# Optimization experiments

Measured on AMD Instinct MI355X. Metric: run time of the kernel, lower is better.

The kernel has to match this reference:

```python
import jax, jax.numpy as jnp
import numpy as np

B, T, DIM, E, H = 128, 512, 256, 512, 512

def _linear_params(key, out_dim, in_dim, bias=True):
    k1, k2 = jax.random.split(key)
    bound = 1.0 / np.sqrt(in_dim)
    W = jax.random.uniform(k1, (out_dim, in_dim), jnp.float32, -bound, bound)
    if bias:
        b = jax.random.uniform(k2, (out_dim,), jnp.float32, -bound, bound)
        return W, b
    return W

def setup_inputs() -> dict:
    key = jax.random.key(0)
    ks = jax.random.split(key, 12)
    x_t = jax.random.normal(ks[0], (B, T, DIM), jnp.float32)
    h0 = jax.random.normal(ks[1], (B, H), jnp.float32)
    c0 = jax.random.normal(ks[2], (B, H), jnp.float32)
    We, be = _linear_params(ks[3], E, DIM)
    Wf, bf = _linear_params(ks[4], H, E)   # forget input proj
    Wi, bi = _linear_params(ks[5], H, E)   # input gate
    Wg, bg = _linear_params(ks[6], H, E)   # cell candidate
    Wo, bo = _linear_params(ks[7], H, E)   # output gate
    Rf = _linear_params(ks[8], H, H, bias=False)
    Ri = _linear_params(ks[9], H, H, bias=False)
    Rg = _linear_params(ks[10], H, H, bias=False)
    Ro = _linear_params(ks[11], H, H, bias=False)
    return dict(x_t=x_t, h0=h0, c0=c0, We=We, be=be,
                Wf=Wf, bf=bf, Wi=Wi, bi=bi, Wg=Wg, bg=bg, Wo=Wo, bo=bo,
                Rf=Rf, Ri=Ri, Rg=Rg, Ro=Ro)

def reference(x_t, h0, c0, We, be, Wf, bf, Wi, bi, Wg, bg, Wo, bo, Rf, Ri, Rg, Ro):
    # Embedding: [B,T,DIM] -> [B,T,E]
    xe = jnp.einsum('btd,ed->bte', x_t, We) + be
    # Batch all input-to-hidden projections across time in one GEMM each.
    xf = jnp.einsum('bte,he->bth', xe, Wf) + bf
    xi = jnp.einsum('bte,he->bth', xe, Wi) + bi
    xg = jnp.einsum('bte,he->bth', xe, Wg) + bg
    xo = jnp.einsum('bte,he->bth', xe, Wo) + bo
    xs = jnp.stack([xi, xf, xg, xo], axis=0)  # [4,B,T,H]

    def step(carry, x4):
        h, c = carry
        xi_t, xf_t, xg_t, xo_t = x4
        i = jax.nn.sigmoid(xi_t + h @ Ri.T)
        f = jax.nn.sigmoid(xf_t + h @ Rf.T)
        g = jnp.tanh(xg_t + h @ Rg.T)
        c_next = g * i + f * c
        o = jax.nn.sigmoid(xo_t + h @ Ro.T)
        h_next = o * jnp.tanh(c_next)
        return (h_next, c_next), h_next

    (h_last, c_last), hs = jax.lax.scan(step, (h0, c0), jnp.moveaxis(xs, 2, 0))
    hidden_seq = jnp.swapaxes(hs, 0, 1)  # [B,T,H]
    return hidden_seq, h_last, c_last
```

## Files before the change

### kernel.cpp

```cpp
#include <hip/hip_runtime.h>
#include <hip/hip_bf16.h>

#define B_ 128
#define T_ 512
#define DIM_ 256
#define E_ 512
#define H_ 512
#define NB_ 32
#define NG_ 8
#define WROW 1032

typedef __attribute__((ext_vector_type(8))) short short8;
typedef __attribute__((ext_vector_type(4))) float floatx4;
typedef unsigned long long ull_t;

__device__ __forceinline__ float sigmoidf_(float x) {
  return 1.0f / (1.0f + __expf(-x));
}

__device__ __forceinline__ short f2bs(float f) {
  __hip_bfloat16 h = __float2bfloat16(f);
  return *reinterpret_cast<short*>(&h);
}

__global__ __launch_bounds__(256) void cvt_we(const float* __restrict__ src,
                                              __hip_bfloat16* __restrict__ dst,
                                              int n) {
  int i = blockIdx.x * 256 + threadIdx.x;
  if (i < n) dst[i] = __float2bfloat16(src[i]);
}

__global__ __launch_bounds__(256) void embed_gemm(
    const float* __restrict__ A,
    const __hip_bfloat16* __restrict__ W,
    const float* __restrict__ bias,
    __hip_bfloat16* __restrict__ C)
{
  const int tid = threadIdx.x;
  const int lane = tid & 63;
  const int w = tid >> 6;
  const int q = lane >> 4;
  const int l15 = lane & 15;
  const int m0 = blockIdx.x * 32 + (w >> 1) * 16;
  const int n0 = (w & 1) * 256;

  const float* a_base = A + (size_t)(m0 + l15) * DIM_ + q * 8;

  floatx4 acc[16];
#pragma unroll
  for (int j = 0; j < 16; ++j) acc[j] = (floatx4){0.f, 0.f, 0.f, 0.f};

  for (int ks = 0; ks < 8; ++ks) {
    const float* ap = a_base + ks * 32;
    short8 a;
#pragma unroll
    for (int j = 0; j < 8; ++j) a[j] = f2bs(ap[j]);
    short8 bf[16];
#pragma unroll
    for (int j = 0; j < 16; ++j) {
      const short* b_ptr =
          (const short*)W + (n0 + j * 16 + l15) * DIM_ + ks * 32 + q * 8;
      bf[j] = *(const short8*)b_ptr;
    }
#pragma unroll
    for (int j = 0; j < 16; ++j)
      acc[j] = __builtin_amdgcn_mfma_f32_16x16x32_bf16(a, bf[j], acc[j], 0, 0, 0);
  }

#pragma unroll
  for (int j = 0; j < 16; ++j) {
    const int col = n0 + j * 16 + l15;
    const float bv = bias[col];
#pragma unroll
    for (int r = 0; r < 4; ++r) {
      const int row = m0 + q * 4 + r;
      C[(size_t)row * E_ + col] = __float2bfloat16(acc[j][r] + bv);
    }
  }
}

__global__ __launch_bounds__(256, 1) void lstm_persist(
    const float* __restrict__ h0,
    const float* __restrict__ c0,
    const float* __restrict__ Wi_, const float* __restrict__ bi_,
    const float* __restrict__ Wf_, const float* __restrict__ bf_,
    const float* __restrict__ Wg_, const float* __restrict__ bg_,
    const float* __restrict__ Wo_, const float* __restrict__ bo_,
    const float* __restrict__ Ri_, const float* __restrict__ Rf_,
    const float* __restrict__ Rg_, const float* __restrict__ Ro_,
    const __hip_bfloat16* __restrict__ xe,
    unsigned* __restrict__ hbuf32,
    unsigned* __restrict__ seq,
    float* __restrict__ out)
{
  extern __shared__ short wts[];
  __shared__ float pbuf[4][4][16][17];
  __shared__ float cbuf[16][16];
  __shared__ float bias_s[4][16];

  const int tid = threadIdx.x;
  const int lane = tid & 63;
  const int w = tid >> 6;
  const int q = lane >> 4;
  const int l15 = lane & 15;
  const int blk = blockIdx.x;
  const int g = blk & 7;
  const int jb = blk >> 3;
  const int b0 = g * 16;
  const int d0 = jb * 16;
  unsigned* seq_g = seq + g * NB_;
  ull_t* hbuf64 = (ull_t*)hbuf32;

  const float* Wp[4] = {Wi_, Wf_, Wg_, Wo_};
  const float* Rp[4] = {Ri_, Rf_, Rg_, Ro_};
  const float* bp[4] = {bi_, bf_, bg_, bo_};

  for (int idx = tid; idx < 64 * 128; idx += 256) {
    const int row = idx >> 7;
    const int ch = idx & 127;
    const int G = row >> 4, dl = row & 15;
    const int k = ch * 8;
    const float* src = (k < 512) ? Wp[G] + (d0 + dl) * E_ + k
                                 : Rp[G] + (d0 + dl) * H_ + (k - 512);
    short8 v;
#pragma unroll
    for (int s = 0; s < 8; ++s) v[s] = f2bs(src[s]);
    *(short8*)&wts[row * WROW + k] = v;
  }
  if (tid < 64) {
    const int G = tid >> 4, n = tid & 15;
    bias_s[G][n] = bp[G][d0 + n];
  }
  {
    const int m = tid >> 4, n = tid & 15;
    cbuf[m][n] = c0[(b0 + m) * H_ + d0 + n];
  }
  if (tid < 128) {
    const int u = g * 4096 + jb * 128 + tid;
    unsigned pk = (unsigned)(unsigned short)f2bs(h0[2 * u]) |
                  ((unsigned)(unsigned short)f2bs(h0[2 * u + 1]) << 16);
    __hip_atomic_store(&hbuf32[u], pk, __ATOMIC_RELAXED,
                       __HIP_MEMORY_SCOPE_AGENT);
  }

  __syncthreads();
  if (tid == 0)
    __hip_atomic_store(&seq_g[jb], 1u, __ATOMIC_RELAXED,
                       __HIP_MEMORY_SCOPE_AGENT);

  const short* xbase = (const short*)xe +
      (size_t)(b0 + l15) * T_ * E_ + w * 256 + q * 8;

  const int lds_base = l15 * WROW + w * 256 + q * 8;

  short8 cur[8];
  if (w < 2) {
#pragma unroll
    for (int s = 0; s < 8; ++s) cur[s] = *(const short8*)(xbase + s * 32);
    floatx4 acc[4];
#pragma unroll
    for (int G = 0; G < 4; ++G) acc[G] = (floatx4){0.f, 0.f, 0.f, 0.f};
#pragma unroll
    for (int s = 0; s < 8; ++s)
#pragma unroll
      for (int G = 0; G < 4; ++G) {
        short8 bfr = *(const short8*)&wts[G * 16 * WROW + lds_base + s * 32];
        acc[G] = __builtin_amdgcn_mfma_f32_16x16x32_bf16(cur[s], bfr, acc[G], 0, 0, 0);
      }
#pragma unroll
    for (int G = 0; G < 4; ++G)
#pragma unroll
      for (int r = 0; r < 4; ++r)
        pbuf[w][G][q * 4 + r][l15] = acc[G][r];
#pragma unroll
    for (int s = 0; s < 8; ++s) cur[s] = *(const short8*)(xbase + E_ + s * 32);
  }

  for (int t = 0; t < T_; ++t) {
    if (w >= 2) {
      const unsigned tgt = (unsigned)(t + 1);
      for (;;) {
        unsigned v = __hip_atomic_load(&seq_g[lane & 31], __ATOMIC_RELAXED,
                                       __HIP_MEMORY_SCOPE_AGENT);
        if (__all((int)(v >= tgt))) break;
      }
      const ull_t* hb = hbuf64 + (size_t)(t & 1) * (B_ * H_ / 4) +
                        (b0 + l15) * (H_ / 4) + (w - 2) * 64 + q * 2;
      short8 hc[8];
#pragma unroll
      for (int s = 0; s < 8; ++s) {
        union { ull_t u[2]; short8 v8; } uu;
        uu.u[0] = __hip_atomic_load(hb + s * 8, __ATOMIC_RELAXED,
                                    __HIP_MEMORY_SCOPE_AGENT);
        uu.u[1] = __hip_atomic_load(hb + s * 8 + 1, __ATOMIC_RELAXED,
                                    __HIP_MEMORY_SCOPE_AGENT);
        hc[s] = uu.v8;
      }
      floatx4 acc[4];
#pragma unroll
      for (int G = 0; G < 4; ++G) acc[G] = (floatx4){0.f, 0.f, 0.f, 0.f};
#pragma unroll
      for (int s = 0; s < 8; ++s)
#pragma unroll
        for (int G = 0; G < 4; ++G) {
          short8 bfr = *(const short8*)&wts[G * 16 * WROW + lds_base + s * 32];
          acc[G] = __builtin_amdgcn_mfma_f32_16x16x32_bf16(hc[s], bfr, acc[G], 0, 0, 0);
        }
#pragma unroll
      for (int G = 0; G < 4; ++G)
#pragma unroll
        for (int r = 0; r < 4; ++r)
          pbuf[w][G][q * 4 + r][l15] = acc[G][r];
    }
    __syncthreads();

    const int m = tid >> 4, n = tid & 15;
    float pre[4];
#pragma unroll
    for (int G = 0; G < 4; ++G)
      pre[G] = pbuf[0][G][m][n] + pbuf[1][G][m][n] + pbuf[2][G][m][n] +
               pbuf[3][G][m][n] + bias_s[G][n];
    const float iv = sigmoidf_(pre[0]);
    const float fv = sigmoidf_(pre[1]);
    const float gv = tanhf(pre[2]);
    const float ov = sigmoidf_(pre[3]);
    const float c = gv * iv + fv * cbuf[m][n];
    cbuf[m][n] = c;
    const float hval = ov * tanhf(c);

    {
      unsigned hv = (unsigned)(unsigned short)f2bs(hval);
      unsigned ov2 = __shfl_xor(hv, 1);
      if ((n & 1) == 0) {
        unsigned pk = hv | (ov2 << 16);
        __hip_atomic_store(
            &hbuf32[((t + 1) & 1) * (B_ * H_ / 2) + (b0 + m) * (H_ / 2) +
                    ((d0 + n) >> 1)],
            pk, __ATOMIC_RELAXED, __HIP_MEMORY_SCOPE_AGENT);
      }
    }
    __syncthreads();
    if (tid == 0)
      __hip_atomic_store(&seq_g[jb], (unsigned)(t + 2), __ATOMIC_RELAXED,
                         __HIP_MEMORY_SCOPE_AGENT);

    out[((size_t)(b0 + m) * T_ + t) * H_ + d0 + n] = hval;
    if (t == T_ - 1) {
      out[(size_t)B_ * T_ * H_ + (b0 + m) * H_ + d0 + n] = hval;
      out[(size_t)B_ * T_ * H_ + B_ * H_ + (b0 + m) * H_ + d0 + n] = c;
    }

    if (w < 2 && t + 1 < T_) {
      floatx4 acc[4];
#pragma unroll
      for (int G = 0; G < 4; ++G) acc[G] = (floatx4){0.f, 0.f, 0.f, 0.f};
#pragma unroll
      for (int s = 0; s < 8; ++s)
#pragma unroll
        for (int G = 0; G < 4; ++G) {
          short8 bfr = *(const short8*)&wts[G * 16 * WROW + lds_base + s * 32];
          acc[G] = __builtin_amdgcn_mfma_f32_16x16x32_bf16(cur[s], bfr, acc[G], 0, 0, 0);
        }
#pragma unroll
      for (int G = 0; G < 4; ++G)
#pragma unroll
        for (int r = 0; r < 4; ++r)
          pbuf[w][G][q * 4 + r][l15] = acc[G][r];
      if (t + 2 < T_) {
        const short* xp = xbase + (size_t)(t + 2) * E_;
#pragma unroll
        for (int s = 0; s < 8; ++s) cur[s] = *(const short8*)(xp + s * 32);
      }
    }
  }
}

extern "C" void kernel_launch(void* const* d_in, const int* in_sizes, int n_in,
                              void* d_out, int out_size, void* d_ws,
                              size_t ws_size, hipStream_t stream) {
  const float* x_t = (const float*)d_in[0];
  const float* h0  = (const float*)d_in[1];
  const float* c0  = (const float*)d_in[2];
  const float* We  = (const float*)d_in[3];
  const float* be  = (const float*)d_in[4];
  const float* Wf  = (const float*)d_in[5];
  const float* bf_ = (const float*)d_in[6];
  const float* Wi  = (const float*)d_in[7];
  const float* bi  = (const float*)d_in[8];
  const float* Wg  = (const float*)d_in[9];
  const float* bg  = (const float*)d_in[10];
  const float* Wo  = (const float*)d_in[11];
  const float* bo  = (const float*)d_in[12];
  const float* Rf  = (const float*)d_in[13];
  const float* Ri  = (const float*)d_in[14];
  const float* Rg  = (const float*)d_in[15];
  const float* Ro  = (const float*)d_in[16];
  float* out = (float*)d_out;

  char* ws = (char*)d_ws;
  unsigned* seq  = (unsigned*)ws;
  unsigned* hbuf = (unsigned*)(ws + 4096);
  __hip_bfloat16* Web  = (__hip_bfloat16*)(ws + 4096 + 262144);
  __hip_bfloat16* xe   = (__hip_bfloat16*)(ws + 4096 + 2 * 262144);

  hipMemsetAsync(seq, 0, 4096, stream);

  cvt_we<<<(E_ * DIM_ + 255) / 256, 256, 0, stream>>>(We, Web, E_ * DIM_);

  embed_gemm<<<(B_ * T_) / 32, 256, 0, stream>>>(x_t, Web, be, xe);

  const size_t lds_bytes = 64 * WROW * sizeof(short);
  lstm_persist<<<NG_ * NB_, 256, lds_bytes, stream>>>(
      h0, c0, Wi, bi, Wf, bf_, Wg, bg, Wo, bo, Ri, Rf, Rg, Ro, xe, hbuf, seq,
      out);
}
```

Measured before the change: 2.281 ms.

## Split K across all four waves and use a per-group counter barrier

Every wave now handles a quarter of both the input projection and the recurrent projection. Before, two waves did only the input part and two did only the recurrent part. The input-projection accumulator is kept in registers and used as the seed for the recurrent MFMAs, which halves the serial recurrent chain per wave on the critical path. Synchronisation moves from per-block sequence flags polled by a wavefront to a single per-group atomic counter polled by thread 0 with s_sleep, followed by a block barrier. This adds an extra __syncthreads per step and atomic contention on one counter. Fast-math sigmoid and tanh are also added, with some accuracy risk.

```diff
diff --git a/kernel.cpp b/kernel.cpp
--- a/kernel.cpp
+++ b/kernel.cpp
@@ -15,7 +15,13 @@
 typedef unsigned long long ull_t;
 
 __device__ __forceinline__ float sigmoidf_(float x) {
-  return 1.0f / (1.0f + __expf(-x));
+  return __fdividef(1.0f, 1.0f + __expf(-x));
+}
+
+__device__ __forceinline__ float tanhf_(float x) {
+  x = fminf(15.0f, fmaxf(-15.0f, x));
+  const float e = __expf(2.0f * x);
+  return __fdividef(e - 1.0f, e + 1.0f);
 }
 
 __device__ __forceinline__ short f2bs(float f) {
@@ -90,7 +96,7 @@
     const float* __restrict__ Rg_, const float* __restrict__ Ro_,
     const __hip_bfloat16* __restrict__ xe,
     unsigned* __restrict__ hbuf32,
-    unsigned* __restrict__ seq,
+    unsigned* __restrict__ cnt,
     float* __restrict__ out)
 {
   extern __shared__ short wts[];
@@ -108,7 +114,7 @@
   const int jb = blk >> 3;
   const int b0 = g * 16;
   const int d0 = jb * 16;
-  unsigned* seq_g = seq + g * NB_;
+  unsigned* cnt_g = cnt + g * 64;
   ull_t* hbuf64 = (ull_t*)hbuf32;
 
   const float* Wp[4] = {Wi_, Wf_, Wg_, Wo_};
@@ -145,73 +151,68 @@
 
   __syncthreads();
   if (tid == 0)
-    __hip_atomic_store(&seq_g[jb], 1u, __ATOMIC_RELAXED,
-                       __HIP_MEMORY_SCOPE_AGENT);
+    __hip_atomic_fetch_add(cnt_g, 1u, __ATOMIC_RELAXED,
+                           __HIP_MEMORY_SCOPE_AGENT);
 
   const short* xbase = (const short*)xe +
-      (size_t)(b0 + l15) * T_ * E_ + w * 256 + q * 8;
-
-  const int lds_base = l15 * WROW + w * 256 + q * 8;
-
-  short8 cur[8];
-  if (w < 2) {
-#pragma unroll
-    for (int s = 0; s < 8; ++s) cur[s] = *(const short8*)(xbase + s * 32);
+      (size_t)(b0 + l15) * T_ * E_ + w * 128 + q * 8;
+  const int lds_w = l15 * WROW + w * 128 + q * 8;
+  const int lds_r = lds_w + 512;
+
+  short8 cur[4];
+  floatx4 accX[4];
+
+#pragma unroll
+  for (int s = 0; s < 4; ++s) cur[s] = *(const short8*)(xbase + s * 32);
+#pragma unroll
+  for (int G = 0; G < 4; ++G) accX[G] = (floatx4){0.f, 0.f, 0.f, 0.f};
+#pragma unroll
+  for (int s = 0; s < 4; ++s)
+#pragma unroll
+    for (int G = 0; G < 4; ++G) {
+      short8 bfr = *(const short8*)&wts[G * 16 * WROW + lds_w + s * 32];
+      accX[G] = __builtin_amdgcn_mfma_f32_16x16x32_bf16(cur[s], bfr, accX[G], 0, 0, 0);
+    }
+#pragma unroll
+  for (int s = 0; s < 4; ++s) cur[s] = *(const short8*)(xbase + E_ + s * 32);
+
+  for (int t = 0; t < T_; ++t) {
+    if (tid == 0) {
+      const unsigned tgt = (unsigned)(NB_ * (t + 1));
+      while (__hip_atomic_load(cnt_g, __ATOMIC_RELAXED,
+                               __HIP_MEMORY_SCOPE_AGENT) < tgt)
+        __builtin_amdgcn_s_sleep(1);
+    }
+    __syncthreads();
+
+    const ull_t* hb = hbuf64 + (size_t)(t & 1) * (B_ * H_ / 4) +
+                      (b0 + l15) * (H_ / 4) + w * 32 + q * 2;
+    short8 hc[4];
+#pragma unroll
+    for (int s = 0; s < 4; ++s) {
+      union { ull_t u[2]; short8 v8; } uu;
+      uu.u[0] = __hip_atomic_load(hb + s * 8, __ATOMIC_RELAXED,
+                                  __HIP_MEMORY_SCOPE_AGENT);
+      uu.u[1] = __hip_atomic_load(hb + s * 8 + 1, __ATOMIC_RELAXED,
+                                  __HIP_MEMORY_SCOPE_AGENT);
+      hc[s] = uu.v8;
+    }
+
     floatx4 acc[4];
 #pragma unroll
-    for (int G = 0; G < 4; ++G) acc[G] = (floatx4){0.f, 0.f, 0.f, 0.f};
-#pragma unroll
-    for (int s = 0; s < 8; ++s)
+    for (int G = 0; G < 4; ++G) acc[G] = accX[G];
+#pragma unroll
+    for (int s = 0; s < 4; ++s)
 #pragma unroll
       for (int G = 0; G < 4; ++G) {
-        short8 bfr = *(const short8*)&wts[G * 16 * WROW + lds_base + s * 32];
-        acc[G] = __builtin_amdgcn_mfma_f32_16x16x32_bf16(cur[s], bfr, acc[G], 0, 0, 0);
+        short8 bfr = *(const short8*)&wts[G * 16 * WROW + lds_r + s * 32];
+        acc[G] = __builtin_amdgcn_mfma_f32_16x16x32_bf16(hc[s], bfr, acc[G], 0, 0, 0);
       }
 #pragma unroll
     for (int G = 0; G < 4; ++G)
 #pragma unroll
       for (int r = 0; r < 4; ++r)
         pbuf[w][G][q * 4 + r][l15] = acc[G][r];
-#pragma unroll
-    for (int s = 0; s < 8; ++s) cur[s] = *(const short8*)(xbase + E_ + s * 32);
-  }
-
-  for (int t = 0; t < T_; ++t) {
-    if (w >= 2) {
-      const unsigned tgt = (unsigned)(t + 1);
-      for (;;) {
-        unsigned v = __hip_atomic_load(&seq_g[lane & 31], __ATOMIC_RELAXED,
-                                       __HIP_MEMORY_SCOPE_AGENT);
-        if (__all((int)(v >= tgt))) break;
-      }
-      const ull_t* hb = hbuf64 + (size_t)(t & 1) * (B_ * H_ / 4) +
-                        (b0 + l15) * (H_ / 4) + (w - 2) * 64 + q * 2;
-      short8 hc[8];
-#pragma unroll
-      for (int s = 0; s < 8; ++s) {
-        union { ull_t u[2]; short8 v8; } uu;
-        uu.u[0] = __hip_atomic_load(hb + s * 8, __ATOMIC_RELAXED,
-                                    __HIP_MEMORY_SCOPE_AGENT);
-        uu.u[1] = __hip_atomic_load(hb + s * 8 + 1, __ATOMIC_RELAXED,
-                                    __HIP_MEMORY_SCOPE_AGENT);
-        hc[s] = uu.v8;
-      }
-      floatx4 acc[4];
-#pragma unroll
-      for (int G = 0; G < 4; ++G) acc[G] = (floatx4){0.f, 0.f, 0.f, 0.f};
-#pragma unroll
-      for (int s = 0; s < 8; ++s)
-#pragma unroll
-        for (int G = 0; G < 4; ++G) {
-          short8 bfr = *(const short8*)&wts[G * 16 * WROW + lds_base + s * 32];
-          acc[G] = __builtin_amdgcn_mfma_f32_16x16x32_bf16(hc[s], bfr, acc[G], 0, 0, 0);
-        }
-#pragma unroll
-      for (int G = 0; G < 4; ++G)
-#pragma unroll
-        for (int r = 0; r < 4; ++r)
-          pbuf[w][G][q * 4 + r][l15] = acc[G][r];
-    }
     __syncthreads();
 
     const int m = tid >> 4, n = tid & 15;
@@ -222,11 +223,11 @@
                pbuf[3][G][m][n] + bias_s[G][n];
     const float iv = sigmoidf_(pre[0]);
     const float fv = sigmoidf_(pre[1]);
-    const float gv = tanhf(pre[2]);
+    const float gv = tanhf_(pre[2]);
     const float ov = sigmoidf_(pre[3]);
-    const float c = gv * iv + fv * cbuf[m][n];
-    cbuf[m][n] = c;
-    const float hval = ov * tanhf(c);
+    const float cv = gv * iv + fv * cbuf[m][n];
+    cbuf[m][n] = cv;
+    const float hval = ov * tanhf_(cv);
 
     {
       unsigned hv = (unsigned)(unsigned short)f2bs(hval);
@@ -241,35 +242,29 @@
     }
     __syncthreads();
     if (tid == 0)
-      __hip_atomic_store(&seq_g[jb], (unsigned)(t + 2), __ATOMIC_RELAXED,
-                         __HIP_MEMORY_SCOPE_AGENT);
+      __hip_atomic_fetch_add(cnt_g, 1u, __ATOMIC_RELAXED,
+                             __HIP_MEMORY_SCOPE_AGENT);
 
     out[((size_t)(b0 + m) * T_ + t) * H_ + d0 + n] = hval;
     if (t == T_ - 1) {
       out[(size_t)B_ * T_ * H_ + (b0 + m) * H_ + d0 + n] = hval;
-      out[(size_t)B_ * T_ * H_ + B_ * H_ + (b0 + m) * H_ + d0 + n] = c;
-    }
-
-    if (w < 2 && t + 1 < T_) {
-      floatx4 acc[4];
-#pragma unroll
-      for (int G = 0; G < 4; ++G) acc[G] = (floatx4){0.f, 0.f, 0.f, 0.f};
-#pragma unroll
-      for (int s = 0; s < 8; ++s)
+      out[(size_t)B_ * T_ * H_ + B_ * H_ + (b0 + m) * H_ + d0 + n] = cv;
+    }
+
+    if (t + 1 < T_) {
+#pragma unroll
+      for (int G = 0; G < 4; ++G) accX[G] = (floatx4){0.f, 0.f, 0.f, 0.f};
+#pragma unroll
+      for (int s = 0; s < 4; ++s)
 #pragma unroll
         for (int G = 0; G < 4; ++G) {
-          short8 bfr = *(const short8*)&wts[G * 16 * WROW + lds_base + s * 32];
-          acc[G] = __builtin_amdgcn_mfma_f32_16x16x32_bf16(cur[s], bfr, acc[G], 0, 0, 0);
+          short8 bfr = *(const short8*)&wts[G * 16 * WROW + lds_w + s * 32];
+          accX[G] = __builtin_amdgcn_mfma_f32_16x16x32_bf16(cur[s], bfr, accX[G], 0, 0, 0);
         }
-#pragma unroll
-      for (int G = 0; G < 4; ++G)
-#pragma unroll
-        for (int r = 0; r < 4; ++r)
-          pbuf[w][G][q * 4 + r][l15] = acc[G][r];
       if (t + 2 < T_) {
         const short* xp = xbase + (size_t)(t + 2) * E_;
 #pragma unroll
-        for (int s = 0; s < 8; ++s) cur[s] = *(const short8*)(xp + s * 32);
+        for (int s = 0; s < 4; ++s) cur[s] = *(const short8*)(xp + s * 32);
       }
     }
   }
@@ -298,12 +293,12 @@
   float* out = (float*)d_out;
 
   char* ws = (char*)d_ws;
-  unsigned* seq  = (unsigned*)ws;
+  unsigned* cnt  = (unsigned*)ws;
   unsigned* hbuf = (unsigned*)(ws + 4096);
   __hip_bfloat16* Web  = (__hip_bfloat16*)(ws + 4096 + 262144);
   __hip_bfloat16* xe   = (__hip_bfloat16*)(ws + 4096 + 2 * 262144);
 
-  hipMemsetAsync(seq, 0, 4096, stream);
+  hipMemsetAsync(cnt, 0, 2048, stream);
 
   cvt_we<<<(E_ * DIM_ + 255) / 256, 256, 0, stream>>>(We, Web, E_ * DIM_);
 
@@ -311,6 +306,6 @@
 
   const size_t lds_bytes = 64 * WROW * sizeof(short);
   lstm_persist<<<NG_ * NB_, 256, lds_bytes, stream>>>(
-      h0, c0, Wi, bi, Wf, bf_, Wg, bg, Wo, bo, Ri, Rf, Rg, Ro, xe, hbuf, seq,
+      h0, c0, Wi, bi, Wf, bf_, Wg, bg, Wo, bo, Ri, Rf, Rg, Ro, xe, hbuf, cnt,
       out);
 }
```

New measurement: 2.039 ms. 1.12x faster.

## Restructure persistent LSTM step sync with padded flags and a single-wave spin

Applied to the files above, without the earlier changes.

Pads the per-block progress flags to separate 128-byte lines so that no two flags share a cache line. Polling moves out of the two h-consuming waves into a single wave that spins after each step, followed by a block barrier. The x-projection MFMA is now issued in the same step as the h-projection instead of one step ahead, and the output store is deferred by one step to take it off the critical path. Fast exp-based tanh and sigmoid replace tanhf and the exact divide. This puts an extra block barrier per step on the critical path and slightly changes numerics.

```diff
diff --git a/kernel.cpp b/kernel.cpp
--- a/kernel.cpp
+++ b/kernel.cpp
@@ -9,13 +9,20 @@
 #define NB_ 32
 #define NG_ 8
 #define WROW 1032
+#define FSTRIDE 32
 
 typedef __attribute__((ext_vector_type(8))) short short8;
 typedef __attribute__((ext_vector_type(4))) float floatx4;
 typedef unsigned long long ull_t;
 
 __device__ __forceinline__ float sigmoidf_(float x) {
-  return 1.0f / (1.0f + __expf(-x));
+  return __fdividef(1.0f, 1.0f + __expf(-x));
+}
+
+__device__ __forceinline__ float tanhf_(float x) {
+  x = fminf(15.0f, fmaxf(-15.0f, x));
+  const float e = __expf(2.0f * x);
+  return __fdividef(e - 1.0f, e + 1.0f);
 }
 
 __device__ __forceinline__ short f2bs(float f) {
@@ -90,7 +97,7 @@
     const float* __restrict__ Rg_, const float* __restrict__ Ro_,
     const __hip_bfloat16* __restrict__ xe,
     unsigned* __restrict__ hbuf32,
-    unsigned* __restrict__ seq,
+    unsigned* __restrict__ flags,
     float* __restrict__ out)
 {
   extern __shared__ short wts[];
@@ -108,7 +115,7 @@
   const int jb = blk >> 3;
   const int b0 = g * 16;
   const int d0 = jb * 16;
-  unsigned* seq_g = seq + g * NB_;
+  unsigned* flags_g = flags + g * (NB_ * FSTRIDE);
   ull_t* hbuf64 = (ull_t*)hbuf32;
 
   const float* Wp[4] = {Wi_, Wf_, Wg_, Wo_};
@@ -145,48 +152,39 @@
 
   __syncthreads();
   if (tid == 0)
-    __hip_atomic_store(&seq_g[jb], 1u, __ATOMIC_RELAXED,
+    __hip_atomic_store(&flags_g[jb * FSTRIDE], 1u, __ATOMIC_RELAXED,
                        __HIP_MEMORY_SCOPE_AGENT);
 
   const short* xbase = (const short*)xe +
       (size_t)(b0 + l15) * T_ * E_ + w * 256 + q * 8;
-
   const int lds_base = l15 * WROW + w * 256 + q * 8;
 
   short8 cur[8];
   if (w < 2) {
 #pragma unroll
     for (int s = 0; s < 8; ++s) cur[s] = *(const short8*)(xbase + s * 32);
-    floatx4 acc[4];
-#pragma unroll
-    for (int G = 0; G < 4; ++G) acc[G] = (floatx4){0.f, 0.f, 0.f, 0.f};
-#pragma unroll
-    for (int s = 0; s < 8; ++s)
-#pragma unroll
-      for (int G = 0; G < 4; ++G) {
-        short8 bfr = *(const short8*)&wts[G * 16 * WROW + lds_base + s * 32];
-        acc[G] = __builtin_amdgcn_mfma_f32_16x16x32_bf16(cur[s], bfr, acc[G], 0, 0, 0);
-      }
-#pragma unroll
-    for (int G = 0; G < 4; ++G)
-#pragma unroll
-      for (int r = 0; r < 4; ++r)
-        pbuf[w][G][q * 4 + r][l15] = acc[G][r];
-#pragma unroll
-    for (int s = 0; s < 8; ++s) cur[s] = *(const short8*)(xbase + E_ + s * 32);
-  }
+  }
+
+  if (w == 3) {
+    unsigned* fp = &flags_g[(lane & 31) * FSTRIDE];
+    for (;;) {
+      unsigned v = __hip_atomic_load(fp, __ATOMIC_RELAXED,
+                                     __HIP_MEMORY_SCOPE_AGENT);
+      if (__all((int)(v >= 1u))) break;
+    }
+  }
+  __syncthreads();
+
+  float hval = 0.f, cv = 0.f;
+  const int m = tid >> 4, n = tid & 15;
 
   for (int t = 0; t < T_; ++t) {
+    if (t > 0)
+      out[((size_t)(b0 + m) * T_ + (t - 1)) * H_ + d0 + n] = hval;
+
     if (w >= 2) {
-      const unsigned tgt = (unsigned)(t + 1);
-      for (;;) {
-        unsigned v = __hip_atomic_load(&seq_g[lane & 31], __ATOMIC_RELAXED,
-                                       __HIP_MEMORY_SCOPE_AGENT);
-        if (__all((int)(v >= tgt))) break;
-      }
       const ull_t* hb = hbuf64 + (size_t)(t & 1) * (B_ * H_ / 4) +
                         (b0 + l15) * (H_ / 4) + (w - 2) * 64 + q * 2;
-      short8 hc[8];
 #pragma unroll
       for (int s = 0; s < 8; ++s) {
         union { ull_t u[2]; short8 v8; } uu;
@@ -194,27 +192,34 @@
                                     __HIP_MEMORY_SCOPE_AGENT);
         uu.u[1] = __hip_atomic_load(hb + s * 8 + 1, __ATOMIC_RELAXED,
                                     __HIP_MEMORY_SCOPE_AGENT);
-        hc[s] = uu.v8;
+        cur[s] = uu.v8;
       }
-      floatx4 acc[4];
-#pragma unroll
-      for (int G = 0; G < 4; ++G) acc[G] = (floatx4){0.f, 0.f, 0.f, 0.f};
-#pragma unroll
-      for (int s = 0; s < 8; ++s)
-#pragma unroll
-        for (int G = 0; G < 4; ++G) {
-          short8 bfr = *(const short8*)&wts[G * 16 * WROW + lds_base + s * 32];
-          acc[G] = __builtin_amdgcn_mfma_f32_16x16x32_bf16(hc[s], bfr, acc[G], 0, 0, 0);
-        }
-#pragma unroll
-      for (int G = 0; G < 4; ++G)
-#pragma unroll
-        for (int r = 0; r < 4; ++r)
-          pbuf[w][G][q * 4 + r][l15] = acc[G][r];
-    }
+    }
+
+    floatx4 acc[4];
+#pragma unroll
+    for (int G = 0; G < 4; ++G) acc[G] = (floatx4){0.f, 0.f, 0.f, 0.f};
+#pragma unroll
+    for (int s = 0; s < 8; ++s)
+#pragma unroll
+      for (int G = 0; G < 4; ++G) {
+        short8 bfr = *(const short8*)&wts[G * 16 * WROW + lds_base + s * 32];
+        acc[G] = __builtin_amdgcn_mfma_f32_16x16x32_bf16(cur[s], bfr, acc[G], 0, 0, 0);
+      }
+
+    if (w < 2 && t + 1 < T_) {
+      const short* xp = xbase + (size_t)(t + 1) * E_;
+#pragma unroll
+      for (int s = 0; s < 8; ++s) cur[s] = *(const short8*)(xp + s * 32);
+    }
+
+#pragma unroll
+    for (int G = 0; G < 4; ++G)
+#pragma unroll
+      for (int r = 0; r < 4; ++r)
+        pbuf[w][G][q * 4 + r][l15] = acc[G][r];
     __syncthreads();
 
-    const int m = tid >> 4, n = tid & 15;
     float pre[4];
 #pragma unroll
     for (int G = 0; G < 4; ++G)
@@ -222,13 +227,13 @@
                pbuf[3][G][m][n] + bias_s[G][n];
     const float iv = sigmoidf_(pre[0]);
     const float fv = sigmoidf_(pre[1]);
-    const float gv = tanhf(pre[2]);
+    const float gv = tanhf_(pre[2]);
     const float ov = sigmoidf_(pre[3]);
-    const float c = gv * iv + fv * cbuf[m][n];
-    cbuf[m][n] = c;
-    const float hval = ov * tanhf(c);
-
-    {
+    cv = gv * iv + fv * cbuf[m][n];
+    cbuf[m][n] = cv;
+    hval = ov * tanhf_(cv);
+
+    if (t + 1 < T_) {
       unsigned hv = (unsigned)(unsigned short)f2bs(hval);
       unsigned ov2 = __shfl_xor(hv, 1);
       if ((n & 1) == 0) {
@@ -238,41 +243,26 @@
                     ((d0 + n) >> 1)],
             pk, __ATOMIC_RELAXED, __HIP_MEMORY_SCOPE_AGENT);
       }
-    }
-    __syncthreads();
-    if (tid == 0)
-      __hip_atomic_store(&seq_g[jb], (unsigned)(t + 2), __ATOMIC_RELAXED,
-                         __HIP_MEMORY_SCOPE_AGENT);
-
-    out[((size_t)(b0 + m) * T_ + t) * H_ + d0 + n] = hval;
-    if (t == T_ - 1) {
-      out[(size_t)B_ * T_ * H_ + (b0 + m) * H_ + d0 + n] = hval;
-      out[(size_t)B_ * T_ * H_ + B_ * H_ + (b0 + m) * H_ + d0 + n] = c;
-    }
-
-    if (w < 2 && t + 1 < T_) {
-      floatx4 acc[4];
-#pragma unroll
-      for (int G = 0; G < 4; ++G) acc[G] = (floatx4){0.f, 0.f, 0.f, 0.f};
-#pragma unroll
-      for (int s = 0; s < 8; ++s)
-#pragma unroll
-        for (int G = 0; G < 4; ++G) {
-          short8 bfr = *(const short8*)&wts[G * 16 * WROW + lds_base + s * 32];
-          acc[G] = __builtin_amdgcn_mfma_f32_16x16x32_bf16(cur[s], bfr, acc[G], 0, 0, 0);
+      __syncthreads();
+      if (tid == 0)
+        __hip_atomic_store(&flags_g[jb * FSTRIDE], (unsigned)(t + 2),
+                           __ATOMIC_RELAXED, __HIP_MEMORY_SCOPE_AGENT);
+      if (w == 3) {
+        unsigned* fp = &flags_g[(lane & 31) * FSTRIDE];
+        const unsigned tgt = (unsigned)(t + 2);
+        for (;;) {
+          unsigned v = __hip_atomic_load(fp, __ATOMIC_RELAXED,
+                                         __HIP_MEMORY_SCOPE_AGENT);
+          if (__all((int)(v >= tgt))) break;
         }
-#pragma unroll
-      for (int G = 0; G < 4; ++G)
-#pragma unroll
-        for (int r = 0; r < 4; ++r)
-          pbuf[w][G][q * 4 + r][l15] = acc[G][r];
-      if (t + 2 < T_) {
-        const short* xp = xbase + (size_t)(t + 2) * E_;
-#pragma unroll
-        for (int s = 0; s < 8; ++s) cur[s] = *(const short8*)(xp + s * 32);
       }
-    }
-  }
+      __syncthreads();
+    }
+  }
+
+  out[((size_t)(b0 + m) * T_ + (T_ - 1)) * H_ + d0 + n] = hval;
+  out[(size_t)B_ * T_ * H_ + (b0 + m) * H_ + d0 + n] = hval;
+  out[(size_t)B_ * T_ * H_ + B_ * H_ + (b0 + m) * H_ + d0 + n] = cv;
 }
 
 extern "C" void kernel_launch(void* const* d_in, const int* in_sizes, int n_in,
@@ -298,12 +288,12 @@
   float* out = (float*)d_out;
 
   char* ws = (char*)d_ws;
-  unsigned* seq  = (unsigned*)ws;
-  unsigned* hbuf = (unsigned*)(ws + 4096);
-  __hip_bfloat16* Web  = (__hip_bfloat16*)(ws + 4096 + 262144);
-  __hip_bfloat16* xe   = (__hip_bfloat16*)(ws + 4096 + 2 * 262144);
-
-  hipMemsetAsync(seq, 0, 4096, stream);
+  unsigned* flags = (unsigned*)ws;
+  unsigned* hbuf  = (unsigned*)(ws + 32768);
+  __hip_bfloat16* Web = (__hip_bfloat16*)(ws + 32768 + 262144);
+  __hip_bfloat16* xe  = (__hip_bfloat16*)(ws + 32768 + 2 * 262144);
+
+  hipMemsetAsync(flags, 0, 32768, stream);
 
   cvt_we<<<(E_ * DIM_ + 255) / 256, 256, 0, stream>>>(We, Web, E_ * DIM_);
 
@@ -311,6 +301,6 @@
 
   const size_t lds_bytes = 64 * WROW * sizeof(short);
   lstm_persist<<<NG_ * NB_, 256, lds_bytes, stream>>>(
-      h0, c0, Wi, bi, Wf, bf_, Wg, bg, Wo, bo, Ri, Rf, Rg, Ro, xe, hbuf, seq,
+      h0, c0, Wi, bi, Wf, bf_, Wg, bg, Wo, bo, Ri, Rf, Rg, Ro, xe, hbuf, flags,
       out);
 }
```

Result: faster. 2.035 ms (-10.8%).
